# Performance work log

Measured on AMD Instinct MI355X. Metric: run time of the kernel, lower is better.

## Reference

```python
import jax, jax.numpy as jnp
import numpy as np

N_NODES = 25000
N_EDGES = 400000
EMBED_DIM = 128
NUM_HEADS = 8
D_K = EMBED_DIM // NUM_HEADS


def setup_inputs() -> dict:
    key = jax.random.key(0)
    ks = jax.random.split(key, 8)
    sc = 1.0 / np.sqrt(EMBED_DIM)
    return {
        "x": jax.random.normal(ks[0], (N_NODES, EMBED_DIM), jnp.float32),
        "edge_index": jax.random.randint(ks[1], (2, N_EDGES), 0, N_NODES),
        "attn_bias": jax.random.normal(ks[2], (N_EDGES, NUM_HEADS), jnp.float32),
        "Wq": jax.random.normal(ks[3], (EMBED_DIM, EMBED_DIM), jnp.float32) * sc,
        "bq": jnp.zeros((EMBED_DIM,), jnp.float32),
        "Wk": jax.random.normal(ks[4], (EMBED_DIM, EMBED_DIM), jnp.float32) * sc,
        "bk": jnp.zeros((EMBED_DIM,), jnp.float32),
        "Wv": jax.random.normal(ks[5], (EMBED_DIM, EMBED_DIM), jnp.float32) * sc,
        "bv": jnp.zeros((EMBED_DIM,), jnp.float32),
        "Wo": jax.random.normal(ks[6], (EMBED_DIM, EMBED_DIM), jnp.float32) * sc,
        "bo": jnp.zeros((EMBED_DIM,), jnp.float32),
    }


def reference(x, edge_index, attn_bias, Wq, bq, Wk, bk, Wv, bv, Wo, bo):
    N = x.shape[0]
    E = edge_index.shape[1]
    H, dk = NUM_HEADS, D_K
    scale = 1.0 / np.sqrt(dk).astype(np.float32)
    dst = edge_index[0]  # query/aggregation node per edge
    src = edge_index[1]  # key/value node per edge

    # project at node level (as torch: linear(x)[index]), then gather per edge
    q = (x @ Wq.T + bq)[dst].reshape(E, H, dk)
    k = (x @ Wk.T + bk)[src].reshape(E, H, dk)
    v = (x @ Wv.T + bv)[src].reshape(E, H, dk)

    logits = scale * jnp.sum(q * k, axis=2) + attn_bias  # [E, H]

    # segment softmax over edges grouped by destination node
    m = jax.ops.segment_max(logits, dst, num_segments=N)     # [N, H]
    e = jnp.exp(logits - m[dst])                              # [E, H]
    z = jax.ops.segment_sum(e, dst, num_segments=N)           # [N, H]
    scores = e / z[dst]                                       # [E, H]

    agg = jax.ops.segment_sum(scores[..., None] * v, dst, num_segments=N)  # [N, H, dk]
    out = agg.reshape(N, H * dk) @ Wo.T + bo                   # [N, embed_dim]
    return out, logits[..., None]
```

## Files before the change

### kernel.cpp

```cpp
#include <hip/hip_runtime.h>
#include <math.h>

#define N_NODES 25000
#define N_EDGES 400000
#define EMBED   128
#define HEADS   8
#define DK      16
#define NBLK    98

typedef __attribute__((ext_vector_type(8))) short bf16x8;
typedef __attribute__((ext_vector_type(4))) float f32x4;
typedef unsigned int uint;
typedef unsigned short ushort;

__device__ inline uint pack2_bf16(float a, float b) {
    union { float f; uint u; } ua, ub;
    ua.f = a; ub.f = b;
    uint ra = (ua.u + 0x7FFFu + ((ua.u >> 16) & 1u)) >> 16;
    uint rb = (ub.u + 0x7FFFu + ((ub.u >> 16) & 1u)) >> 16;
    return (ra & 0xFFFFu) | (rb << 16);
}
__device__ inline ushort cvt_bf16(float a) {
    union { float f; uint u; } ua; ua.f = a;
    return (ushort)((ua.u + 0x7FFFu + ((ua.u >> 16) & 1u)) >> 16);
}
__device__ inline float bf16_lo(uint u) {
    union { uint u; float f; } x; x.u = u << 16; return x.f;
}
__device__ inline float bf16_hi(uint u) {
    union { uint u; float f; } x; x.u = u & 0xFFFF0000u; return x.f;
}

#define NX (N_NODES * 128)
__global__ __launch_bounds__(256) void convert_all(
    const float* __restrict__ x,
    const float* __restrict__ Wq, const float* __restrict__ Wk,
    const float* __restrict__ Wv, const float* __restrict__ Wo,
    ushort* __restrict__ xb, ushort* __restrict__ wb, int* __restrict__ deg)
{
    int i = blockIdx.x * 256 + threadIdx.x;
    if (i < N_NODES) deg[i] = 0;
    int base = i * 2;
    if (base < NX) {
        float2 v = *reinterpret_cast<const float2*>(x + base);
        reinterpret_cast<uint*>(xb)[i] = pack2_bf16(v.x, v.y);
    } else {
        int j = base - NX;
        if (j < 4 * 16384) {
            const float* src = (j < 16384) ? Wq + j
                             : (j < 32768) ? Wk + (j - 16384)
                             : (j < 49152) ? Wv + (j - 32768)
                             :               Wo + (j - 49152);
            float2 v = *reinterpret_cast<const float2*>(src);
            reinterpret_cast<uint*>(wb)[j >> 1] = pack2_bf16(v.x, v.y);
        }
    }
}

__global__ __launch_bounds__(256) void gemm_qkv_deg(
    const ushort* __restrict__ A, const ushort* __restrict__ Wall,
    const float* __restrict__ bq, const float* __restrict__ bk,
    const float* __restrict__ bv,
    ushort* __restrict__ Qb, ushort* __restrict__ Kb, ushort* __restrict__ Vb,
    const int* __restrict__ ei, int* __restrict__ deg,
    int M)
{
    const int which = blockIdx.y;
    if (which == 3) {
        int t = blockIdx.x * 256 + threadIdx.x;
        int e = t * 4;
        if (e + 3 < N_EDGES) {
            int4 d = *reinterpret_cast<const int4*>(ei + e);
            atomicAdd(&deg[d.x], 1);
            atomicAdd(&deg[d.y], 1);
            atomicAdd(&deg[d.z], 1);
            atomicAdd(&deg[d.w], 1);
        } else {
            for (; e < N_EDGES && e < t * 4 + 4; ++e)
                atomicAdd(&deg[ei[e]], 1);
        }
        return;
    }

    const ushort* W = Wall + which * 16384;
    const float* bias = (which == 0) ? bq : (which == 1) ? bk : bv;
    ushort* C = (which == 0) ? Qb : (which == 1) ? Kb : Vb;

    const int lane = threadIdx.x & 63;
    const int wave = threadIdx.x >> 6;
    const int ml   = lane & 15;
    const int quad = lane >> 4;
    const int m0   = blockIdx.x * 64 + wave * 16;

    int arow = m0 + ml; if (arow >= M) arow = M - 1;
    const ushort* ap = A + arow * 128 + quad * 8;

    f32x4 acc[8];
#pragma unroll
    for (int ct = 0; ct < 8; ++ct) acc[ct] = (f32x4){0.f, 0.f, 0.f, 0.f};

#pragma unroll
    for (int ks = 0; ks < 128; ks += 32) {
        bf16x8 af = *reinterpret_cast<const bf16x8*>(ap + ks);
#pragma unroll
        for (int ct = 0; ct < 8; ++ct) {
            bf16x8 bf = *reinterpret_cast<const bf16x8*>(
                W + (ct * 16 + ml) * 128 + ks + quad * 8);
            acc[ct] = __builtin_amdgcn_mfma_f32_16x16x32_bf16(af, bf, acc[ct], 0, 0, 0);
        }
    }

#pragma unroll
    for (int ct = 0; ct < 8; ++ct) {
        int col = ct * 16 + ml;
        float bv_ = bias[col];
#pragma unroll
        for (int r = 0; r < 4; ++r) {
            int row = m0 + quad * 4 + r;
            if (row < M)
                C[row * 128 + col] = cvt_bf16(acc[ct][r] + bv_);
        }
    }
}

__global__ __launch_bounds__(256) void gemm_out(
    const ushort* __restrict__ A, const ushort* __restrict__ W,
    const float* __restrict__ bias, float* __restrict__ C, int M)
{
    const int lane = threadIdx.x & 63;
    const int wave = threadIdx.x >> 6;
    const int ml   = lane & 15;
    const int quad = lane >> 4;
    const int m0   = blockIdx.x * 64 + wave * 16;

    int arow = m0 + ml; if (arow >= M) arow = M - 1;
    const ushort* ap = A + arow * 128 + quad * 8;

    f32x4 acc[8];
#pragma unroll
    for (int ct = 0; ct < 8; ++ct) acc[ct] = (f32x4){0.f, 0.f, 0.f, 0.f};

#pragma unroll
    for (int ks = 0; ks < 128; ks += 32) {
        bf16x8 af = *reinterpret_cast<const bf16x8*>(ap + ks);
#pragma unroll
        for (int ct = 0; ct < 8; ++ct) {
            bf16x8 bf = *reinterpret_cast<const bf16x8*>(
                W + (ct * 16 + ml) * 128 + ks + quad * 8);
            acc[ct] = __builtin_amdgcn_mfma_f32_16x16x32_bf16(af, bf, acc[ct], 0, 0, 0);
        }
    }

#pragma unroll
    for (int ct = 0; ct < 8; ++ct) {
        int col = ct * 16 + ml;
        float bv_ = bias[col];
#pragma unroll
        for (int r = 0; r < 4; ++r) {
            int row = m0 + quad * 4 + r;
            if (row < M)
                C[row * 128 + col] = acc[ct][r] + bv_;
        }
    }
}

__global__ __launch_bounds__(256) void scan_blocks(
    const int* __restrict__ deg, int* __restrict__ excl, int* __restrict__ bsum)
{
    __shared__ int sh[256];
    int t = threadIdx.x;
    int gid = blockIdx.x * 256 + t;
    int v = (gid < N_NODES) ? deg[gid] : 0;
    sh[t] = v;
    __syncthreads();
#pragma unroll
    for (int off = 1; off < 256; off <<= 1) {
        int u = (t >= off) ? sh[t - off] : 0;
        __syncthreads();
        sh[t] += u;
        __syncthreads();
    }
    if (gid < N_NODES) excl[gid] = sh[t] - v;
    if (t == 255) bsum[blockIdx.x] = sh[255];
}

__global__ __launch_bounds__(128) void scan_tops(
    const int* __restrict__ bsum, int* __restrict__ bbase)
{
    __shared__ int sh[128];
    int t = threadIdx.x;
    int v = (t < NBLK) ? bsum[t] : 0;
    sh[t] = v;
    __syncthreads();
#pragma unroll
    for (int off = 1; off < 128; off <<= 1) {
        int u = (t >= off) ? sh[t - off] : 0;
        __syncthreads();
        sh[t] += u;
        __syncthreads();
    }
    if (t < NBLK) bbase[t] = sh[t] - v;
}

__global__ __launch_bounds__(256) void scan_apply(
    int* __restrict__ excl, const int* __restrict__ bbase,
    int* __restrict__ cursor)
{
    int t = threadIdx.x;
    int gid = blockIdx.x * 256 + t;
    if (gid < N_NODES) {
        int o = excl[gid] + bbase[blockIdx.x];
        excl[gid] = o;
        cursor[gid] = o;
    }
    if (blockIdx.x == 0 && t == 0) excl[N_NODES] = N_EDGES;
}

__global__ __launch_bounds__(256) void scatter_edges(
    const int* __restrict__ ei, int* __restrict__ cursor,
    int2* __restrict__ csr2)
{
    int e = blockIdx.x * 256 + threadIdx.x;
    if (e >= N_EDGES) return;
    int dst = ei[e];
    int src = ei[N_EDGES + e];
    int pos = atomicAdd(&cursor[dst], 1);
    csr2[pos] = make_int2(e, src);
}

__global__ __launch_bounds__(256) void fused_attn(
    const ushort* __restrict__ Q2, const ushort* __restrict__ K2,
    const ushort* __restrict__ V2,
    const float* __restrict__ attn_bias,
    const int* __restrict__ offsets, const int2* __restrict__ csr2,
    float* __restrict__ logits, ushort* __restrict__ AGG)
{
    const int lane = threadIdx.x & 63;
    const int wid  = threadIdx.x >> 6;
    const int n = blockIdx.x * 4 + wid;
    const int start = offsets[n], end = offsets[n + 1];
    const int h  = lane & 7;
    const int es = lane >> 3;

    const uint4* Qu4 = reinterpret_cast<const uint4*>(Q2);
    const uint4* Ku4 = reinterpret_cast<const uint4*>(K2);
    const uint4* Vu4 = reinterpret_cast<const uint4*>(V2);

    uint4 qa = Qu4[n * 16 + h * 2];
    uint4 qb = Qu4[n * 16 + h * 2 + 1];
    float qf[16];
    {
        uint qq[8] = {qa.x, qa.y, qa.z, qa.w, qb.x, qb.y, qb.z, qb.w};
#pragma unroll
        for (int j = 0; j < 8; ++j) {
            qf[2 * j]     = bf16_lo(qq[j]);
            qf[2 * j + 1] = bf16_hi(qq[j]);
        }
    }

    float acc[16];
#pragma unroll
    for (int j = 0; j < 16; ++j) acc[j] = 0.f;
    float z = 0.f;

    for (int base = start; base < end; base += 8) {
        bool valid = (base + es) < end;
        int idx = base + es; if (!valid) idx = end - 1;
        int2 epair = csr2[idx];
        int e = epair.x, s = epair.y;

        uint4 k0 = Ku4[s * 16 + h * 2];
        uint4 k1 = Ku4[s * 16 + h * 2 + 1];
        uint4 v0 = Vu4[s * 16 + h * 2];
        uint4 v1 = Vu4[s * 16 + h * 2 + 1];
        float bias = attn_bias[e * 8 + h];

        uint kk[8] = {k0.x, k0.y, k0.z, k0.w, k1.x, k1.y, k1.z, k1.w};
        float d = 0.f;
#pragma unroll
        for (int j = 0; j < 8; ++j)
            d += qf[2 * j] * bf16_lo(kk[j]) + qf[2 * j + 1] * bf16_hi(kk[j]);

        float l = 0.25f * d + bias;
        float p = 0.f;
        if (valid) {
            logits[e * 8 + h] = l;
            p = __expf(l);
        }
        z += p;

        uint vv[8] = {v0.x, v0.y, v0.z, v0.w, v1.x, v1.y, v1.z, v1.w};
#pragma unroll
        for (int j = 0; j < 8; ++j) {
            acc[2 * j]     += p * bf16_lo(vv[j]);
            acc[2 * j + 1] += p * bf16_hi(vv[j]);
        }
    }

    {
        int bit = (lane >> 5) & 1;
#pragma unroll
        for (int j = 0; j < 8; ++j) {
            float send = bit ? acc[j] : acc[j + 8];
            float keep = bit ? acc[j + 8] : acc[j];
            acc[j] = keep + __shfl_xor(send, 32, 64);
        }
        bit = (lane >> 4) & 1;
#pragma unroll
        for (int j = 0; j < 4; ++j) {
            float send = bit ? acc[j] : acc[j + 4];
            float keep = bit ? acc[j + 4] : acc[j];
            acc[j] = keep + __shfl_xor(send, 16, 64);
        }
        bit = (lane >> 3) & 1;
#pragma unroll
        for (int j = 0; j < 2; ++j) {
            float send = bit ? acc[j] : acc[j + 2];
            float keep = bit ? acc[j + 2] : acc[j];
            acc[j] = keep + __shfl_xor(send, 8, 64);
        }
    }
    z += __shfl_xor(z, 8, 64);
    z += __shfl_xor(z, 16, 64);
    z += __shfl_xor(z, 32, 64);

    float inv = (z > 0.f) ? 1.f / z : 0.f;
    int d_off = ((lane >> 5) & 1) * 8 + ((lane >> 4) & 1) * 4 + ((lane >> 3) & 1) * 2;
    reinterpret_cast<uint*>(AGG)[n * 64 + h * 8 + (d_off >> 1)] =
        pack2_bf16(acc[0] * inv, acc[1] * inv);
}

extern "C" void kernel_launch(void* const* d_in, const int* in_sizes, int n_in,
                              void* d_out, int out_size, void* d_ws, size_t ws_size,
                              hipStream_t stream)
{
    const float* x         = (const float*)d_in[0];
    const int*   ei        = (const int*)  d_in[1];
    const float* attn_bias = (const float*)d_in[2];
    const float* Wq = (const float*)d_in[3];
    const float* bq = (const float*)d_in[4];
    const float* Wk = (const float*)d_in[5];
    const float* bk = (const float*)d_in[6];
    const float* Wv = (const float*)d_in[7];
    const float* bv = (const float*)d_in[8];
    const float* Wo = (const float*)d_in[9];
    const float* bo = (const float*)d_in[10];

    float* out    = (float*)d_out;
    float* logits = out + N_NODES * EMBED;

    ushort* xb   = (ushort*)d_ws;
    ushort* wb   = xb + NX;
    ushort* Qb   = wb + 4 * 16384;
    ushort* Kb   = Qb + NX;
    ushort* Vb   = Kb + NX;
    ushort* AGGb = Vb + NX;
    int* deg     = (int*)(AGGb + NX);
    int* offsets = deg + N_NODES;
    int* cursor  = offsets + N_NODES + 1;
    int2* csr2   = (int2*)(cursor + N_NODES);
    int* bsum    = (int*)(csr2 + N_EDGES);
    int* bbase   = bsum + NBLK;

    int npairs = (NX + 4 * 16384) / 2;
    convert_all<<<(npairs + 255) / 256, 256, 0, stream>>>(x, Wq, Wk, Wv, Wo, xb, wb, deg);

    int gblocks = (N_NODES + 63) / 64;
    dim3 qkvgrid(gblocks, 4);
    gemm_qkv_deg<<<qkvgrid, 256, 0, stream>>>(xb, wb, bq, bk, bv, Qb, Kb, Vb,
                                              ei, deg, N_NODES);

    scan_blocks<<<NBLK, 256, 0, stream>>>(deg, offsets, bsum);
    scan_tops<<<1, 128, 0, stream>>>(bsum, bbase);
    scan_apply<<<NBLK, 256, 0, stream>>>(offsets, bbase, cursor);
    scatter_edges<<<(N_EDGES + 255) / 256, 256, 0, stream>>>(ei, cursor, csr2);

    fused_attn<<<N_NODES / 4, 256, 0, stream>>>(Qb, Kb, Vb, attn_bias,
                                                offsets, csr2, logits, AGGb);

    gemm_out<<<gblocks, 256, 0, stream>>>(AGGb, wb + 3 * 16384, bo, out, N_NODES);
}
```

Measured before the change: 210.1 us.

## Fuse Q/K/V projections per wave and fold scan_tops into scan_apply

The QKV GEMM now has one 64-thread wave compute all three projections for a 16-row tile, so each A fragment is loaded once and reused across Wq, Wk and Wv. The launch grid becomes 1563x2, with the y=1 blocks still doing the degree counting. The separate single-block top-level scan kernel is removed: each scan_apply block sums the preceding block totals itself with a wave reduction, saving one launch. The trade-off is more accumulator registers per thread (24 MFMA tiles) and smaller blocks in the GEMM.

```diff
diff --git a/kernel.cpp b/kernel.cpp
--- a/kernel.cpp
+++ b/kernel.cpp
@@ -7,6 +7,7 @@
 #define HEADS   8
 #define DK      16
 #define NBLK    98
+#define GQB     1563
 
 typedef __attribute__((ext_vector_type(8))) short bf16x8;
 typedef __attribute__((ext_vector_type(4))) float f32x4;
@@ -57,7 +58,7 @@
     }
 }
 
-__global__ __launch_bounds__(256) void gemm_qkv_deg(
+__global__ __launch_bounds__(64) void gemm_qkv3(
     const ushort* __restrict__ A, const ushort* __restrict__ Wall,
     const float* __restrict__ bq, const float* __restrict__ bk,
     const float* __restrict__ bv,
@@ -65,9 +66,8 @@
     const int* __restrict__ ei, int* __restrict__ deg,
     int M)
 {
-    const int which = blockIdx.y;
-    if (which == 3) {
-        int t = blockIdx.x * 256 + threadIdx.x;
+    if (blockIdx.y == 1) {
+        int t = blockIdx.x * 64 + threadIdx.x;
         int e = t * 4;
         if (e + 3 < N_EDGES) {
             int4 d = *reinterpret_cast<const int4*>(ei + e);
@@ -82,43 +82,47 @@
         return;
     }
 
-    const ushort* W = Wall + which * 16384;
-    const float* bias = (which == 0) ? bq : (which == 1) ? bk : bv;
-    ushort* C = (which == 0) ? Qb : (which == 1) ? Kb : Vb;
-
-    const int lane = threadIdx.x & 63;
-    const int wave = threadIdx.x >> 6;
+    const int lane = threadIdx.x;
     const int ml   = lane & 15;
     const int quad = lane >> 4;
-    const int m0   = blockIdx.x * 64 + wave * 16;
+    const int m0   = blockIdx.x * 16;
 
     int arow = m0 + ml; if (arow >= M) arow = M - 1;
     const ushort* ap = A + arow * 128 + quad * 8;
 
-    f32x4 acc[8];
-#pragma unroll
-    for (int ct = 0; ct < 8; ++ct) acc[ct] = (f32x4){0.f, 0.f, 0.f, 0.f};
+    f32x4 acc[24];
+#pragma unroll
+    for (int i = 0; i < 24; ++i) acc[i] = (f32x4){0.f, 0.f, 0.f, 0.f};
 
 #pragma unroll
     for (int ks = 0; ks < 128; ks += 32) {
         bf16x8 af = *reinterpret_cast<const bf16x8*>(ap + ks);
 #pragma unroll
+        for (int w = 0; w < 3; ++w) {
+#pragma unroll
+            for (int ct = 0; ct < 8; ++ct) {
+                bf16x8 bf = *reinterpret_cast<const bf16x8*>(
+                    Wall + w * 16384 + (ct * 16 + ml) * 128 + ks + quad * 8);
+                acc[w * 8 + ct] =
+                    __builtin_amdgcn_mfma_f32_16x16x32_bf16(af, bf, acc[w * 8 + ct], 0, 0, 0);
+            }
+        }
+    }
+
+#pragma unroll
+    for (int w = 0; w < 3; ++w) {
+        ushort* C = (w == 0) ? Qb : (w == 1) ? Kb : Vb;
+        const float* bias = (w == 0) ? bq : (w == 1) ? bk : bv;
+#pragma unroll
         for (int ct = 0; ct < 8; ++ct) {
-            bf16x8 bf = *reinterpret_cast<const bf16x8*>(
-                W + (ct * 16 + ml) * 128 + ks + quad * 8);
-            acc[ct] = __builtin_amdgcn_mfma_f32_16x16x32_bf16(af, bf, acc[ct], 0, 0, 0);
-        }
-    }
-
-#pragma unroll
-    for (int ct = 0; ct < 8; ++ct) {
-        int col = ct * 16 + ml;
-        float bv_ = bias[col];
-#pragma unroll
-        for (int r = 0; r < 4; ++r) {
-            int row = m0 + quad * 4 + r;
-            if (row < M)
-                C[row * 128 + col] = cvt_bf16(acc[ct][r] + bv_);
+            int col = ct * 16 + ml;
+            float bv_ = bias[col];
+#pragma unroll
+            for (int r = 0; r < 4; ++r) {
+                int row = m0 + quad * 4 + r;
+                if (row < M)
+                    C[row * 128 + col] = cvt_bf16(acc[w * 8 + ct][r] + bv_);
+            }
         }
     }
 }
@@ -184,32 +188,23 @@
     if (t == 255) bsum[blockIdx.x] = sh[255];
 }
 
-__global__ __launch_bounds__(128) void scan_tops(
-    const int* __restrict__ bsum, int* __restrict__ bbase)
-{
-    __shared__ int sh[128];
+__global__ __launch_bounds__(256) void scan_apply(
+    int* __restrict__ excl, const int* __restrict__ bsum,
+    int* __restrict__ cursor)
+{
+    __shared__ int base_sh;
     int t = threadIdx.x;
-    int v = (t < NBLK) ? bsum[t] : 0;
-    sh[t] = v;
+    if (t < 64) {
+        int s = 0;
+        for (int i = t; i < (int)blockIdx.x; i += 64) s += bsum[i];
+#pragma unroll
+        for (int off = 32; off; off >>= 1) s += __shfl_xor(s, off, 64);
+        if (t == 0) base_sh = s;
+    }
     __syncthreads();
-#pragma unroll
-    for (int off = 1; off < 128; off <<= 1) {
-        int u = (t >= off) ? sh[t - off] : 0;
-        __syncthreads();
-        sh[t] += u;
-        __syncthreads();
-    }
-    if (t < NBLK) bbase[t] = sh[t] - v;
-}
-
-__global__ __launch_bounds__(256) void scan_apply(
-    int* __restrict__ excl, const int* __restrict__ bbase,
-    int* __restrict__ cursor)
-{
-    int t = threadIdx.x;
     int gid = blockIdx.x * 256 + t;
     if (gid < N_NODES) {
-        int o = excl[gid] + bbase[blockIdx.x];
+        int o = excl[gid] + base_sh;
         excl[gid] = o;
         cursor[gid] = o;
     }
@@ -360,23 +355,21 @@
     int* cursor  = offsets + N_NODES + 1;
     int2* csr2   = (int2*)(cursor + N_NODES);
     int* bsum    = (int*)(csr2 + N_EDGES);
-    int* bbase   = bsum + NBLK;
 
     int npairs = (NX + 4 * 16384) / 2;
     convert_all<<<(npairs + 255) / 256, 256, 0, stream>>>(x, Wq, Wk, Wv, Wo, xb, wb, deg);
 
-    int gblocks = (N_NODES + 63) / 64;
-    dim3 qkvgrid(gblocks, 4);
-    gemm_qkv_deg<<<qkvgrid, 256, 0, stream>>>(xb, wb, bq, bk, bv, Qb, Kb, Vb,
-                                              ei, deg, N_NODES);
+    dim3 qkvgrid(GQB, 2);
+    gemm_qkv3<<<qkvgrid, 64, 0, stream>>>(xb, wb, bq, bk, bv, Qb, Kb, Vb,
+                                          ei, deg, N_NODES);
 
     scan_blocks<<<NBLK, 256, 0, stream>>>(deg, offsets, bsum);
-    scan_tops<<<1, 128, 0, stream>>>(bsum, bbase);
-    scan_apply<<<NBLK, 256, 0, stream>>>(offsets, bbase, cursor);
+    scan_apply<<<NBLK, 256, 0, stream>>>(offsets, bsum, cursor);
     scatter_edges<<<(N_EDGES + 255) / 256, 256, 0, stream>>>(ei, cursor, csr2);
 
     fused_attn<<<N_NODES / 4, 256, 0, stream>>>(Qb, Kb, Vb, attn_bias,
                                                 offsets, csr2, logits, AGGb);
 
+    int gblocks = (N_NODES + 63) / 64;
     gemm_out<<<gblocks, 256, 0, stream>>>(AGGb, wb + 3 * 16384, bo, out, N_NODES);
 }
```

After: 222.8 us. 1.06x slower.
